# Kernel optimization log

Measured on AMD Instinct MI355X. Metric: run time of the kernel, lower is better.

## Reference

```python
import jax, jax.numpy as jnp
import numpy as np

N, E, C, Z, NB, NG, NL = 4000, 48000, 64, 10, 8, 8, 2
R_MAX = 5.0
P = 5.0  # polynomial cutoff power
AVG_NEIGH = 12.0
# l-index of each of the 16 spherical-harmonic components (l = 0..3)
ELLS = np.concatenate([[0], [1] * 3, [2] * 5, [3] * 7])


def _sph(u):
    # component-normalized real spherical harmonics up to l=3, u: unit vectors [E,3]
    x, y, z = u[..., 0], u[..., 1], u[..., 2]
    s3 = np.sqrt(3.0); s5 = np.sqrt(5.0); s15 = np.sqrt(15.0)
    s7 = np.sqrt(7.0); s105 = np.sqrt(105.0)
    s35_8 = np.sqrt(35.0 / 8.0); s21_8 = np.sqrt(21.0 / 8.0)
    x2, y2, z2 = x * x, y * y, z * z
    return jnp.stack([
        jnp.ones_like(x),
        s3 * x, s3 * y, s3 * z,
        s15 * x * y, s15 * y * z, 0.5 * s5 * (3.0 * z2 - 1.0), s15 * x * z, 0.5 * s15 * (x2 - y2),
        s35_8 * y * (3.0 * x2 - y2), s105 * x * y * z, s21_8 * y * (5.0 * z2 - 1.0),
        0.5 * s7 * z * (5.0 * z2 - 3.0), s21_8 * x * (5.0 * z2 - 1.0),
        0.5 * s105 * z * (x2 - y2), s35_8 * x * (x2 - 3.0 * y2),
    ], axis=-1)


def _radial(r):
    # Bessel radial basis * polynomial cutoff envelope; r: [E,1] -> [E,NB]
    n = jnp.arange(1, NB + 1, dtype=r.dtype)
    bess = np.sqrt(2.0 / R_MAX) * jnp.sin(n * jnp.pi * r / R_MAX) / r
    u = r / R_MAX
    env = 1.0 - 0.5 * (P + 1) * (P + 2) * u ** P + P * (P + 2) * u ** (P + 1) - 0.5 * P * (P + 1) * u ** (P + 2)
    env = jnp.where(u < 1.0, env, 0.0)
    return bess * env


def _per_l(f, W):
    # per-degree (l) channel mixing: f [N,C,16], W [4,C,C]
    return jnp.einsum('ncm,mcd->ndm', f, W[ELLS])


def _model(positions, x, shifts, W_embed, W_up, Wm1, Wm2, Wm3, W_out, W_sc, a_sc, w_poly, W_prod, w_r0, W_r1, w_r2, edge_index, batch):
    sender, receiver = edge_index[0], edge_index[1]
    vec = positions[receiver] - positions[sender] + shifts          # [E,3]
    length = jnp.sqrt(jnp.sum(vec * vec, axis=-1, keepdims=True))   # [E,1]
    edge_attrs = _sph(vec / length)                                 # [E,16]
    edge_feats = _radial(length)                                    # [E,NB]
    nf = jnp.zeros((N, C, 16), positions.dtype).at[:, :, 0].set(x @ W_embed)
    node_e = jnp.zeros((N,), positions.dtype)
    for i in range(NL):
        h = _per_l(nf, W_up[i])                                     # [N,C,16]
        w = jax.nn.silu(edge_feats @ Wm1[i])
        w = jax.nn.silu(w @ Wm2[i])
        w = (w @ Wm3[i]).reshape(E, C, 4)                           # per-(channel,l) radial weights
        h_s = h[:, :, 0][sender][:, :, None]                        # sender scalar feats [E,C,1]
        m = w[:, :, ELLS] * edge_attrs[:, None, :] * h_s            # messages [E,C,16]
        agg = jax.ops.segment_sum(m, receiver, num_segments=N) / AVG_NEIGH
        out = _per_l(agg, W_out[i])
        sc = _per_l(nf, W_sc[i]) * (x @ a_sc[i])[:, :, None]        # element-dependent skip
        s = out[:, :, 0]
        gate = w_poly[i, 0] + w_poly[i, 1] * s + w_poly[i, 2] * s * s  # correlation-3 scalar gate
        nf = _per_l(out * gate[:, :, None], W_prod[i]) + sc
        if i < NL - 1:
            node_e = node_e + nf[:, :, 0] @ w_r0
        else:
            node_e = node_e + jax.nn.silu(nf[:, :, 0] @ W_r1) @ w_r2
    snap = jax.ops.segment_sum(node_e, batch, num_segments=NG)
    return snap, node_e


def setup_inputs() -> dict:
    key = jax.random.key(0)
    ks = jax.random.split(key, 20)
    positions = jax.random.normal(ks[0], (N, 3), jnp.float32) * 3.0
    species = jax.random.randint(ks[1], (N,), 0, Z)
    x = jax.nn.one_hot(species, Z, dtype=jnp.float32)
    sender = jax.random.randint(ks[2], (E,), 0, N)
    offset = jax.random.randint(ks[3], (E,), 1, N)
    receiver = (sender + offset) % N  # no self loops -> length > 0
    edge_index = jnp.stack([sender, receiver]).astype(jnp.int32)
    shifts = jnp.zeros((E, 3), jnp.float32)
    batch = jnp.sort(jax.random.randint(ks[4], (N,), 0, NG)).astype(jnp.int32)
    g = lambda k, shp, scale: jax.random.normal(k, shp, jnp.float32) * scale
    inv = 1.0 / np.sqrt(C)
    return {
        'positions': positions, 'x': x, 'shifts': shifts,
        'W_embed': g(ks[5], (Z, C), 1.0 / np.sqrt(Z)),
        'W_up': g(ks[6], (NL, 4, C, C), inv),
        'Wm1': g(ks[7], (NL, NB, 64), 1.0 / np.sqrt(NB)),
        'Wm2': g(ks[8], (NL, 64, 64), 0.125),
        'Wm3': g(ks[9], (NL, 64, 4 * C), 0.125),
        'W_out': g(ks[10], (NL, 4, C, C), inv),
        'W_sc': g(ks[11], (NL, 4, C, C), inv),
        'a_sc': g(ks[12], (NL, Z, C), 1.0),
        'w_poly': g(ks[13], (NL, 3, C), 0.5),
        'W_prod': g(ks[14], (NL, 4, C, C), inv),
        'w_r0': g(ks[15], (C,), inv),
        'W_r1': g(ks[16], (C, 16), inv),
        'w_r2': g(ks[17], (16,), 0.25),
        'edge_index': edge_index, 'batch': batch,
    }


def reference(positions, x, shifts, W_embed, W_up, Wm1, Wm2, Wm3, W_out, W_sc, a_sc, w_poly, W_prod, w_r0, W_r1, w_r2, edge_index, batch):
    def efn(pos):
        snap, node_e = _model(pos, x, shifts, W_embed, W_up, Wm1, Wm2, Wm3, W_out, W_sc, a_sc, w_poly, W_prod, w_r0, W_r1, w_r2, edge_index, batch)
        return jnp.sum(snap), (snap, node_e)
    (_, (snap, node_e)), g = jax.value_and_grad(efn, has_aux=True)(positions)
    forces = -g
    return snap, node_e, forces
```

## Files before the change

kernel.cpp:

```cpp
#include <hip/hip_runtime.h>
#include <math.h>

constexpr int NN = 4000;
constexpr int EE = 48000;
constexpr int ZZ = 10;
constexpr float RMAX = 5.0f;
constexpr float INV_AVG = 1.0f / 12.0f;

constexpr int GB_EDGE = 188;
constexpr int GB_SPEC = GB_EDGE + 16;
constexpr int GB_W3Z  = GB_SPEC + 32;
constexpr int GB_T0   = GB_W3Z + 3;
constexpr int GB_ZERO = GB_T0 + 64;
constexpr int ZWS_F4  = 3*NN*64/4;
constexpr int ZOUT_F4 = 3*NN/4;

__device__ __forceinline__ float rl(float v, int lane){
    return __uint_as_float(__builtin_amdgcn_readlane(__float_as_uint(v), lane));
}
__device__ __forceinline__ float sigf(float x){ return 1.0f/(1.0f+__expf(-x)); }
__device__ __forceinline__ float siluf(float x){ return x*sigf(x); }
__device__ __forceinline__ float dsiluf(float x){ float s=sigf(x); return s*(1.0f+x*(1.0f-s)); }

__device__ __forceinline__ void pin64(float (&W)[64]){
#pragma unroll
    for (int i=0;i<64;i++) asm volatile("" : "+v"(W[i]));
}
__device__ __forceinline__ void pin8(float (&W)[8]){
#pragma unroll
    for (int i=0;i<8;i++) asm volatile("" : "+v"(W[i]));
}

__device__ __forceinline__ float bmv64(float src, const float (&W)[64]){
    float a0=0.f,a1=0.f,a2=0.f,a3=0.f;
#pragma unroll
    for (int k=0;k<64;k+=4){
        a0 += rl(src,k+0)*W[k+0];
        a1 += rl(src,k+1)*W[k+1];
        a2 += rl(src,k+2)*W[k+2];
        a3 += rl(src,k+3)*W[k+3];
    }
    return (a0+a1)+(a2+a3);
}
__device__ __forceinline__ void load_row64(const float* __restrict__ p, float (&W)[64]){
#pragma unroll
    for (int i=0;i<16;i++){
        float4 v = reinterpret_cast<const float4*>(p)[i];
        W[4*i]=v.x; W[4*i+1]=v.y; W[4*i+2]=v.z; W[4*i+3]=v.w;
    }
}
__device__ __forceinline__ void load_col64(const float* __restrict__ p, int lane, float (&W)[64]){
#pragma unroll
    for (int k=0;k<64;k++) W[k] = p[k*64+lane];
}

__global__ void k_zero(int* __restrict__ ecount, float* __restrict__ out)
{
    int t = threadIdx.x;
    if (t < 8) out[t] = 0.0f;
    if (t == 8) *ecount = 0;
}

__global__ void k_geom(const float* __restrict__ pos, const float* __restrict__ shifts,
                       const int* __restrict__ ei, const float* __restrict__ x,
                       const float* __restrict__ WE, const float* __restrict__ W_up,
                       const float* __restrict__ W_sc, const float* __restrict__ a_sc,
                       const float* __restrict__ Wm3,
                       int* __restrict__ spec,
                       float* __restrict__ u3c, float* __restrict__ frc, float* __restrict__ dfrc,
                       int* __restrict__ esrc, int* __restrict__ edst, int* __restrict__ ecount,
                       float* __restrict__ T0, float* __restrict__ SC0, float* __restrict__ W3z,
                       float4* __restrict__ zws, float* __restrict__ out)
{
    int b = blockIdx.x;
    if (b >= GB_T0){
        if (b >= GB_ZERO) return;
        if (b >= GB_W3Z && b < GB_T0){}
        if (b >= GB_T0 && b < GB_ZERO){
            float4 z4 = make_float4(0.f,0.f,0.f,0.f);
            float4* zout = (float4*)(out + 8 + NN);
            for (int i=(b-GB_T0)*256 + threadIdx.x; i < ZWS_F4 + ZOUT_F4; i += 64*256){
                if (i < ZWS_F4) zws[i] = z4;
                else zout[i-ZWS_F4] = z4;
            }
            return;
        }
    }
    if (b >= GB_W3Z && b < GB_T0){
        int wv = (b-GB_W3Z)*4 + (threadIdx.x>>6);
        int lane = threadIdx.x & 63;
        if (wv < ZZ){
            float wev = WE[wv*64 + lane];
            float t=0.f, sc=0.f;
#pragma unroll
            for (int c=0;c<64;c++){
                float w = rl(wev,c);
                t  += w*W_up[c*64+lane];
                sc += w*W_sc[c*64+lane];
            }
            T0[wv*64+lane]  = t;
            SC0[wv*64+lane] = sc * a_sc[wv*64+lane];
        }
        return;
    }
    if (b >= GB_SPEC && b < GB_W3Z){
        int idx = (b-GB_SPEC)*256 + threadIdx.x;
        int l = idx >> 12;
        int kc = idx & 4095;
        int k = kc >> 6, c = kc & 63;
        W3z[idx] = Wm3[l*64*256 + k*256 + 4*c];
        return;
    }
    if (b >= GB_EDGE){
        int n = (b-GB_EDGE)*256 + threadIdx.x;
        if (n < NN){
            int sp = 0;
#pragma unroll
            for (int j=0;j<ZZ;j++) if (x[n*ZZ+j] > 0.5f) sp = j;
            spec[n] = sp;
        }
        return;
    }
    int e = b*256 + threadIdx.x;
    if (e >= EE) return;
    int s = ei[e], r = ei[EE+e];
    float vx = pos[r*3+0]-pos[s*3+0]+shifts[e*3+0];
    float vy = pos[r*3+1]-pos[s*3+1]+shifts[e*3+1];
    float vz = pos[r*3+2]-pos[s*3+2]+shifts[e*3+2];
    float rr = sqrtf(vx*vx+vy*vy+vz*vz);
    float u = rr*(1.0f/RMAX);
    if (u >= 1.0f) return;
    int slot = atomicAdd(ecount, 1);
    esrc[slot]=s; edst[slot]=r;
    float inv = 1.0f/rr;
    u3c[slot*3+0]=vx*inv; u3c[slot*3+1]=vy*inv; u3c[slot*3+2]=vz*inv;
    float u2=u*u, u4=u2*u2, u5=u4*u;
    float env  = 1.0f - 21.0f*u5 + 35.0f*u5*u - 15.0f*u5*u2;
    float om   = 1.0f-u;
    float denv = -21.0f*u4*om*om;
    const float A = 0.6324555320336759f;
    const float K1 = 3.14159265358979f/RMAX;
    float a  = K1*rr;
    float s1 = __sinf(a), c1 = __cosf(a);
    float sp = 0.0f, cp = 1.0f, sn = s1, cn = c1;
#pragma unroll
    for (int n=1;n<=8;n++){
        float k = (float)n*K1;
        float bess  = A*sn*inv;
        float dbess = A*(k*cn - sn*inv)*inv;
        frc [slot*8+n-1] = bess*env;
        dfrc[slot*8+n-1] = dbess*env + bess*denv;
        float s2 = 2.0f*c1*sn - sp; sp=sn; sn=s2;
        float c2 = 2.0f*c1*cn - cp; cp=cn; cn=c2;
    }
}

template<int L>
__global__ __launch_bounds__(256,3)
void k_edge_fwd(const float* __restrict__ frc, const int* __restrict__ esrc,
                const int* __restrict__ edst, const int* __restrict__ ecount,
                const int* __restrict__ spec, const float* __restrict__ T0,
                const float* __restrict__ h1,
                const float* __restrict__ W1, const float* __restrict__ W2,
                const float* __restrict__ W3z,
                float* __restrict__ agg, float* __restrict__ t2b,
                float* __restrict__ w0b)
{
    int lane = threadIdx.x & 63;
    int wid  = __builtin_amdgcn_readfirstlane((blockIdx.x*256 + threadIdx.x) >> 6);
    const int nw = 512*4;
    int cnt  = ecount[0];
    float W1c[8], W2c[64], W3c[64];
#pragma unroll
    for (int j=0;j<8;j++) W1c[j] = W1[j*64+lane];
    load_col64(W2,  lane, W2c);
    load_col64(W3z, lane, W3c);
    pin8(W1c); pin64(W2c); pin64(W3c);
    for (int slot=wid; slot<cnt; slot+=nw){
        int us = __builtin_amdgcn_readfirstlane(slot);
        int s = esrc[us], r = edst[us];
        float fv = frc[us*8 + (lane&7)];
        float t1=0.f;
#pragma unroll
        for (int j=0;j<8;j++) t1 += rl(fv,j)*W1c[j];
        float a1v = siluf(t1);
        float t2  = bmv64(a1v, W2c);
        float a2v = siluf(t2);
        float w0  = bmv64(a2v, W3c);
        if (L==1){
            t2b[(size_t)us*64+lane] = t2;
            w0b[(size_t)us*64+lane] = w0;
        }
        float h = (L==0) ? T0[spec[s]*64+lane] : h1[s*64+lane];
        atomicAdd(&agg[r*64+lane], w0*h*INV_AVG);
    }
}

__global__ __launch_bounds__(256,2)
void k_node_fwd0(const float* __restrict__ agg, const float* __restrict__ SC0,
                 const int* __restrict__ spec, const int* __restrict__ batch,
                 const float* __restrict__ Wout, const float* __restrict__ Wprod,
                 const float* __restrict__ Wup1, const float* __restrict__ poly,
                 const float* __restrict__ wr0,
                 float* __restrict__ s0, float* __restrict__ nf1,
                 float* __restrict__ h1, float* __restrict__ out)
{
    __shared__ float part[8];
    if (threadIdx.x < 8) part[threadIdx.x] = 0.f;
    __syncthreads();
    int lane = threadIdx.x & 63;
    int wid = __builtin_amdgcn_readfirstlane((blockIdx.x*256 + threadIdx.x) >> 6);
    float WA[64], WB[64], WC[64];
    load_col64(Wout, lane, WA);
    load_col64(Wprod,lane, WB);
    load_col64(Wup1, lane, WC);
    pin64(WA); pin64(WB); pin64(WC);
    float p0=poly[lane], p1=poly[64+lane], p2=poly[128+lane];
    float w0r = wr0[lane];
#pragma unroll
    for (int i=0;i<4;i++){
        int n = wid + i*1000;
        float av = agg[n*64+lane];
        float s  = bmv64(av, WA);
        float gate = p0 + p1*s + p2*s*s;
        float nf = bmv64(s*gate, WB) + SC0[spec[n]*64+lane];
        s0 [n*64+lane] = s;
        nf1[n*64+lane] = nf;
        h1 [n*64+lane] = bmv64(nf, WC);
        float ne = nf*w0r;
#pragma unroll
        for (int off=32;off;off>>=1) ne += __shfl_xor(ne,off);
        if (lane==0){ out[8+n] = ne; atomicAdd(&part[batch[n]], ne); }
    }
    __syncthreads();
    if (threadIdx.x < 8) atomicAdd(&out[threadIdx.x], part[threadIdx.x]);
}

__global__ __launch_bounds__(256,2)
void k_node1(const float* __restrict__ agg, const float* __restrict__ nf1,
             const int* __restrict__ spec, const int* __restrict__ batch,
             const float* __restrict__ Wout, const float* __restrict__ Wprod,
             const float* __restrict__ Wsc, const float* __restrict__ asc,
             const float* __restrict__ poly, const float* __restrict__ Wr1,
             const float* __restrict__ wr2,
             float* __restrict__ out, float* __restrict__ gagg, float* __restrict__ gacc)
{
    __shared__ float part[8];
    if (threadIdx.x < 8) part[threadIdx.x] = 0.f;
    __syncthreads();
    int lane = threadIdx.x & 63;
    int wid = __builtin_amdgcn_readfirstlane((blockIdx.x*256 + threadIdx.x) >> 6);
    float WA[64], WB[64], WC[64];
    float sA[4], nfA[4], gA[4]; int spA[4];
    float p0=poly[lane], p1=poly[64+lane], p2=poly[128+lane];
    load_col64(Wout, lane, WA);
    load_col64(Wprod,lane, WB);
    load_col64(Wsc,  lane, WC);
    pin64(WA); pin64(WB); pin64(WC);
#pragma unroll
    for (int i=0;i<4;i++){
        int n = wid + i*1000;
        spA[i] = spec[n];
        float av  = agg[n*64+lane];
        float nfv = nf1[n*64+lane];
        float s   = bmv64(av, WA);
        float gate = p0 + p1*s + p2*s*s;
        float scp = bmv64(nfv, WC);
        sA[i]  = s;
        nfA[i] = bmv64(s*gate, WB) + scp*asc[spA[i]*64+lane];
    }
    int j = lane & 15;
    float w2 = wr2[j];
#pragma unroll
    for (int c=0;c<64;c++) WA[c] = Wr1[c*16 + j];
    pin64(WA);
#pragma unroll
    for (int i2=0;i2<4;i2++){
        float4 v = reinterpret_cast<const float4*>(Wr1 + lane*16)[i2];
        WC[4*i2]=v.x; WC[4*i2+1]=v.y; WC[4*i2+2]=v.z; WC[4*i2+3]=v.w;
    }
#pragma unroll
    for (int i=0;i<4;i++){
        int n = wid + i*1000;
        float z  = bmv64(nfA[i], WA);
        float ne = siluf(z)*w2;
#pragma unroll
        for (int off=32;off;off>>=1) ne += __shfl_xor(ne,off);
        ne *= 0.25f;
        float gz = w2*dsiluf(z);
        float g = 0.f;
#pragma unroll
        for (int jj=0;jj<16;jj++) g += rl(gz,jj)*WC[jj];
        gA[i] = g;
        if (lane==0){ out[8+n] += ne; atomicAdd(&part[batch[n]], ne); }
    }
    load_row64(Wprod + lane*64, WA);
    load_row64(Wout  + lane*64, WB);
    load_row64(Wsc   + lane*64, WC);
    pin64(WA); pin64(WB); pin64(WC);
#pragma unroll
    for (int i=0;i<4;i++){
        int n = wid + i*1000;
        float g  = gA[i];
        float gv = bmv64(g, WA);
        float s  = sA[i];
        float gate = p0 + p1*s + p2*s*s;
        float gs = gv*(gate + s*(p1 + 2.0f*p2*s));
        gagg[n*64+lane] = bmv64(gs, WB);
        gacc[n*64+lane] = bmv64(g*asc[spA[i]*64+lane], WC);
    }
    __syncthreads();
    if (threadIdx.x < 8) atomicAdd(&out[threadIdx.x], part[threadIdx.x]);
}

__global__ __launch_bounds__(256,2)
void k_bnode0(const float* __restrict__ ghb, const float* __restrict__ gacc,
              const float* __restrict__ Wup1, const float* __restrict__ wr0,
              const float* __restrict__ sbuf, const float* __restrict__ Wout,
              const float* __restrict__ Wprod, const float* __restrict__ poly,
              float* __restrict__ gagg)
{
    int lane = threadIdx.x & 63;
    int wid = __builtin_amdgcn_readfirstlane((blockIdx.x*256 + threadIdx.x) >> 6);
    float WA[64], WB[64], WC[64];
    load_row64(Wup1 + lane*64, WA);
    load_row64(Wprod+ lane*64, WB);
    load_row64(Wout + lane*64, WC);
    pin64(WA); pin64(WB); pin64(WC);
    float p0=poly[lane], p1=poly[64+lane], p2=poly[128+lane];
    float w0r = wr0[lane];
#pragma unroll
    for (int i=0;i<4;i++){
        int n = wid + i*1000;
        float gh = ghb[n*64+lane];
        float g  = bmv64(gh, WA) + gacc[n*64+lane] + w0r;
        float gv = bmv64(g, WB);
        float s  = sbuf[n*64+lane];
        float gate = p0 + p1*s + p2*s*s;
        float gs = gv*(gate + s*(p1 + 2.0f*p2*s));
        gagg[n*64+lane] = bmv64(gs, WC);
    }
}

__global__ __launch_bounds__(256,3)
void k_edge_bwd1(const float* __restrict__ frc, const float* __restrict__ dfrc,
                 const float* __restrict__ u3c, const int* __restrict__ esrc,
                 const int* __restrict__ edst, const int* __restrict__ ecount,
                 const float* __restrict__ h1, const float* __restrict__ gagg,
                 const float* __restrict__ t2b, const float* __restrict__ w0b,
                 const float* __restrict__ W1, const float* __restrict__ W2,
                 const float* __restrict__ W3z,
                 float* __restrict__ ghb, float* __restrict__ out)
{
    int lane = threadIdx.x & 63;
    int wid  = __builtin_amdgcn_readfirstlane((blockIdx.x*256 + threadIdx.x) >> 6);
    const int nw = 512*4;
    int cnt  = ecount[0];
    float* outf = out + 8 + NN;
    float W3r[64], W2r[64], W1c[8];
    load_row64(W3z + lane*64, W3r);
    load_row64(W2  + lane*64, W2r);
#pragma unroll
    for (int j=0;j<8;j++) W1c[j] = W1[j*64+lane];
    pin64(W3r); pin64(W2r); pin8(W1c);
    for (int slot=wid; slot<cnt; slot+=nw){
        int us = __builtin_amdgcn_readfirstlane(slot);
        int s = esrc[us], r = edst[us];
        float gm = gagg[r*64+lane]*INV_AVG;
        float h  = h1[s*64+lane];
        atomicAdd(&ghb[s*64+lane], gm*w0b[(size_t)us*64+lane]);
        float ga2 = bmv64(gm*h, W3r);
        float gt2 = ga2*dsiluf(t2b[(size_t)us*64+lane]);
        float ga1 = bmv64(gt2, W2r);
        float fv  = frc [us*8+(lane&7)];
        float dfv = dfrc[us*8+(lane&7)];
        float t1=0.f, wd=0.f;
#pragma unroll
        for (int j=0;j<8;j++){ t1 += rl(fv,j)*W1c[j]; wd += rl(dfv,j)*W1c[j]; }
        float p = ga1*dsiluf(t1)*wd;
#pragma unroll
        for (int off=32;off;off>>=1) p += __shfl_xor(p,off);
        if (lane<3) atomicAdd(&outf[r*3+lane], -u3c[us*3+lane]*p);
        else if (lane>=32 && lane<35){ int d=lane-32; atomicAdd(&outf[s*3+d], u3c[us*3+d]*p); }
    }
}

__global__ __launch_bounds__(256,2)
void k_edge_bwd0(const float* __restrict__ frc, const float* __restrict__ dfrc,
                 const float* __restrict__ u3c, const int* __restrict__ esrc,
                 const int* __restrict__ edst, const int* __restrict__ ecount,
                 const int* __restrict__ spec, const float* __restrict__ T0,
                 const float* __restrict__ gagg,
                 const float* __restrict__ W1, const float* __restrict__ W2,
                 const float* __restrict__ W3z,
                 float* __restrict__ out)
{
    int lane = threadIdx.x & 63;
    int wid  = __builtin_amdgcn_readfirstlane((blockIdx.x*256 + threadIdx.x) >> 6);
    const int nw = 512*4;
    int cnt  = ecount[0];
    float* outf = out + 8 + NN;
    float W3r[64], W2r[64], W2c[64], W1c[8];
    load_row64(W3z + lane*64, W3r);
    load_row64(W2  + lane*64, W2r);
    load_col64(W2, lane, W2c);
#pragma unroll
    for (int j=0;j<8;j++) W1c[j] = W1[j*64+lane];
    pin64(W3r); pin64(W2r); pin64(W2c); pin8(W1c);
    for (int slot=wid; slot<cnt; slot+=nw){
        int us = __builtin_amdgcn_readfirstlane(slot);
        int s = esrc[us], r = edst[us];
        float gm = gagg[r*64+lane]*INV_AVG;
        float h  = T0[spec[s]*64+lane];
        float ga2 = bmv64(gm*h, W3r);
        float fv  = frc [us*8+(lane&7)];
        float dfv = dfrc[us*8+(lane&7)];
        float t1=0.f, wd=0.f;
#pragma unroll
        for (int j=0;j<8;j++){ t1 += rl(fv,j)*W1c[j]; wd += rl(dfv,j)*W1c[j]; }
        float a1v = siluf(t1);
        float t2  = bmv64(a1v, W2c);
        float gt2 = ga2*dsiluf(t2);
        float ga1 = bmv64(gt2, W2r);
        float p = ga1*dsiluf(t1)*wd;
#pragma unroll
        for (int off=32;off;off>>=1) p += __shfl_xor(p,off);
        if (lane<3) atomicAdd(&outf[r*3+lane], -u3c[us*3+lane]*p);
        else if (lane>=32 && lane<35){ int d=lane-32; atomicAdd(&outf[s*3+d], u3c[us*3+d]*p); }
    }
}

extern "C" void kernel_launch(void* const* d_in, const int* in_sizes, int n_in,
                              void* d_out, int out_size, void* d_ws, size_t ws_size,
                              hipStream_t stream)
{
    (void)in_sizes; (void)n_in; (void)out_size; (void)ws_size;
    const float* pos    = (const float*)d_in[0];
    const float* x      = (const float*)d_in[1];
    const float* shifts = (const float*)d_in[2];
    const float* W_embed= (const float*)d_in[3];
    const float* W_up   = (const float*)d_in[4];
    const float* Wm1    = (const float*)d_in[5];
    const float* Wm2    = (const float*)d_in[6];
    const float* Wm3    = (const float*)d_in[7];
    const float* W_out  = (const float*)d_in[8];
    const float* W_sc   = (const float*)d_in[9];
    const float* a_sc   = (const float*)d_in[10];
    const float* w_poly = (const float*)d_in[11];
    const float* W_prod = (const float*)d_in[12];
    const float* w_r0   = (const float*)d_in[13];
    const float* W_r1   = (const float*)d_in[14];
    const float* w_r2   = (const float*)d_in[15];
    const int*   ei     = (const int*)d_in[16];
    const int*   batch  = (const int*)d_in[17];
    float* out = (float*)d_out;

    float* F = (float*)d_ws;
    float* agg0 = F; F += NN*64;
    float* agg1 = F; F += NN*64;
    float* ghb  = F; F += NN*64;
    int* ecount = (int*)F; F += 4;
    float* u3c  = F; F += 3*EE;
    float* frc  = F; F += 8*EE;
    float* dfrc = F; F += 8*EE;
    float* t2b1 = F; F += (size_t)EE*64;
    float* w0b1 = F; F += (size_t)EE*64;
    float* h1   = F; F += NN*64;
    float* nf1  = F; F += NN*64;
    float* s0   = F; F += NN*64;
    float* gagg1= F; F += NN*64;
    float* gagg0= F; F += NN*64;
    float* gacc = F; F += NN*64;
    float* T0   = F; F += ZZ*64;
    float* SC0  = F; F += ZZ*64;
    float* W3z  = F; F += 2*64*64;
    int* spec   = (int*)F; F += NN;
    int* esrc   = (int*)F; F += EE;
    int* edst   = (int*)F; F += EE;

    const float* U0 = W_up;           const float* U1 = W_up   + 4*64*64;
    const float* O0 = W_out;          const float* O1 = W_out  + 4*64*64;
    const float* S0w= W_sc;           const float* S1w= W_sc   + 4*64*64;
    const float* P0 = W_prod;         const float* P1 = W_prod + 4*64*64;
    const float* M1_0=Wm1,  *M1_1=Wm1+8*64;
    const float* M2_0=Wm2,  *M2_1=Wm2+64*64;
    const float* asc1=a_sc+ZZ*64;
    const float* pl0=w_poly, *pl1=w_poly+3*64;
    float* W3z0 = W3z; float* W3z1 = W3z + 64*64;

    k_zero<<<1, 256, 0, stream>>>(ecount, out);
    k_geom<<<GB_ZERO, 256, 0, stream>>>(pos, shifts, ei, x, W_embed, U0, S0w, a_sc, Wm3,
                                        spec, u3c, frc, dfrc, esrc, edst, ecount,
                                        T0, SC0, W3z, (float4*)d_ws, out);

    k_edge_fwd<0><<<512,256,0,stream>>>(frc, esrc, edst, ecount, spec, T0, nullptr,
                                        M1_0, M2_0, W3z0, agg0, nullptr, nullptr);
    k_node_fwd0<<<250,256,0,stream>>>(agg0, SC0, spec, batch, O0, P0, U1, pl0, w_r0,
                                      s0, nf1, h1, out);
    k_edge_fwd<1><<<512,256,0,stream>>>(frc, esrc, edst, ecount, spec, nullptr, h1,
                                        M1_1, M2_1, W3z1, agg1, t2b1, w0b1);
    k_node1<<<250,256,0,stream>>>(agg1, nf1, spec, batch, O1, P1, S1w, asc1, pl1,
                                  W_r1, w_r2, out, gagg1, gacc);

    k_edge_bwd1<<<512,256,0,stream>>>(frc, dfrc, u3c, esrc, edst, ecount, h1,
                                      gagg1, t2b1, w0b1, M1_1, M2_1, W3z1, ghb, out);
    k_bnode0<<<250,256,0,stream>>>(ghb, gacc, U1, w_r0, s0, O0, P0, pl0, gagg0);
    k_edge_bwd0<<<512,256,0,stream>>>(frc, dfrc, u3c, esrc, edst, ecount, spec, T0,
                                      gagg0, M1_0, M2_0, W3z0, out);
}
```

Before: 159.3 us.

## Fuse all stages into one persistent kernel with software grid barriers

Replaces the sequence of nine launches (geometry, two forward edge passes, node passes, backward edge and node passes) with a single persistent 512-block kernel. Stages are separated by atomic-counter grid barriers instead of kernel boundaries. The layer-0 t2 activations are now also stored so the backward pass can reuse them. This is meant to remove launch gaps and tail idle time between the many short stages. In exchange it relies on all 512 blocks being co-resident, forces launch bounds of 2 blocks per CU, and adds barrier spin cost and extra memory traffic for the stored activations.

```diff
diff --git a/kernel.cpp b/kernel.cpp
--- a/kernel.cpp
+++ b/kernel.cpp
@@ -7,11 +7,13 @@
 constexpr float RMAX = 5.0f;
 constexpr float INV_AVG = 1.0f / 12.0f;
 
-constexpr int GB_EDGE = 188;
-constexpr int GB_SPEC = GB_EDGE + 16;
-constexpr int GB_W3Z  = GB_SPEC + 32;
-constexpr int GB_T0   = GB_W3Z + 3;
-constexpr int GB_ZERO = GB_T0 + 64;
+constexpr int GRID  = 512;
+constexpr int NWAVE = GRID * 4;
+
+constexpr int RB_SPEC = 188;
+constexpr int RB_W3Z  = 204;
+constexpr int RB_T0   = 236;
+constexpr int RB_ZERO = 239;
 constexpr int ZWS_F4  = 3*NN*64/4;
 constexpr int ZOUT_F4 = 3*NN/4;
 
@@ -30,7 +32,6 @@
 #pragma unroll
     for (int i=0;i<8;i++) asm volatile("" : "+v"(W[i]));
 }
-
 __device__ __forceinline__ float bmv64(float src, const float (&W)[64]){
     float a0=0.f,a1=0.f,a2=0.f,a3=0.f;
 #pragma unroll
@@ -54,379 +55,375 @@
     for (int k=0;k<64;k++) W[k] = p[k*64+lane];
 }
 
-__global__ void k_zero(int* __restrict__ ecount, float* __restrict__ out)
+__device__ __forceinline__ void gbar(int* __restrict__ bc, int id){
+    __syncthreads();
+    if (threadIdx.x == 0){
+        __threadfence();
+        __hip_atomic_fetch_add(bc + id*64, 1, __ATOMIC_RELEASE, __HIP_MEMORY_SCOPE_AGENT);
+        while (__hip_atomic_load(bc + id*64, __ATOMIC_ACQUIRE, __HIP_MEMORY_SCOPE_AGENT) < GRID)
+            __builtin_amdgcn_s_sleep(1);
+        __threadfence();
+    }
+    __syncthreads();
+}
+
+__global__ void k_zero(int* __restrict__ barcnt, int* __restrict__ ecount, float* __restrict__ out)
 {
     int t = threadIdx.x;
+    barcnt[t] = 0; barcnt[t+256] = 0;
+    if (t == 0) *ecount = 0;
     if (t < 8) out[t] = 0.0f;
-    if (t == 8) *ecount = 0;
-}
-
-__global__ void k_geom(const float* __restrict__ pos, const float* __restrict__ shifts,
-                       const int* __restrict__ ei, const float* __restrict__ x,
-                       const float* __restrict__ WE, const float* __restrict__ W_up,
-                       const float* __restrict__ W_sc, const float* __restrict__ a_sc,
-                       const float* __restrict__ Wm3,
-                       int* __restrict__ spec,
-                       float* __restrict__ u3c, float* __restrict__ frc, float* __restrict__ dfrc,
-                       int* __restrict__ esrc, int* __restrict__ edst, int* __restrict__ ecount,
-                       float* __restrict__ T0, float* __restrict__ SC0, float* __restrict__ W3z,
-                       float4* __restrict__ zws, float* __restrict__ out)
+}
+
+__global__ __launch_bounds__(256,2)
+void k_main(const float* __restrict__ pos, const float* __restrict__ shifts,
+            const int* __restrict__ ei, const float* __restrict__ x,
+            const float* __restrict__ WE, const float* __restrict__ W_up,
+            const float* __restrict__ Wm1, const float* __restrict__ Wm2,
+            const float* __restrict__ Wm3, const float* __restrict__ W_out,
+            const float* __restrict__ W_sc, const float* __restrict__ a_sc,
+            const float* __restrict__ w_poly, const float* __restrict__ W_prod,
+            const float* __restrict__ w_r0, const float* __restrict__ W_r1,
+            const float* __restrict__ w_r2, const int* __restrict__ batch,
+            int* __restrict__ spec, float* __restrict__ u3c,
+            float* __restrict__ frc, float* __restrict__ dfrc,
+            int* __restrict__ esrc, int* __restrict__ edst, int* __restrict__ ecount,
+            float* __restrict__ T0, float* __restrict__ SC0, float* __restrict__ W3z,
+            float* __restrict__ agg0, float* __restrict__ agg1, float* __restrict__ ghb,
+            float* __restrict__ t2b0, float* __restrict__ t2b1, float* __restrict__ w0b1,
+            float* __restrict__ h1b, float* __restrict__ nf1b, float* __restrict__ s0b,
+            float* __restrict__ gagg0, float* __restrict__ gagg1, float* __restrict__ gacc,
+            int* __restrict__ barcnt, float4* __restrict__ zws,
+            float* __restrict__ out)
 {
-    int b = blockIdx.x;
-    if (b >= GB_T0){
-        if (b >= GB_ZERO) return;
-        if (b >= GB_W3Z && b < GB_T0){}
-        if (b >= GB_T0 && b < GB_ZERO){
-            float4 z4 = make_float4(0.f,0.f,0.f,0.f);
-            float4* zout = (float4*)(out + 8 + NN);
-            for (int i=(b-GB_T0)*256 + threadIdx.x; i < ZWS_F4 + ZOUT_F4; i += 64*256){
-                if (i < ZWS_F4) zws[i] = z4;
-                else zout[i-ZWS_F4] = z4;
+    __shared__ float part[8];
+    const int bid  = blockIdx.x;
+    const int tid  = threadIdx.x;
+    const int lane = tid & 63;
+    const int gw   = bid*4 + (tid>>6);
+
+    const float* U0  = W_up;          const float* U1  = W_up   + 16384;
+    const float* O0  = W_out;         const float* O1  = W_out  + 16384;
+    const float* S0w = W_sc;          const float* S1w = W_sc   + 16384;
+    const float* P0w = W_prod;        const float* P1w = W_prod + 16384;
+    const float* M1_0= Wm1;           const float* M1_1= Wm1 + 512;
+    const float* M2_0= Wm2;           const float* M2_1= Wm2 + 4096;
+    const float* asc1= a_sc + ZZ*64;
+    const float* pl0 = w_poly;        const float* pl1 = w_poly + 192;
+    const float* W3z0= W3z;           const float* W3z1= W3z + 4096;
+    float* outf = out + 8 + NN;
+
+    if (bid < RB_SPEC){
+        int e = bid*256 + tid;
+        if (e < EE){
+            int s = ei[e], r = ei[EE+e];
+            float vx = pos[r*3+0]-pos[s*3+0]+shifts[e*3+0];
+            float vy = pos[r*3+1]-pos[s*3+1]+shifts[e*3+1];
+            float vz = pos[r*3+2]-pos[s*3+2]+shifts[e*3+2];
+            float rr = sqrtf(vx*vx+vy*vy+vz*vz);
+            float u = rr*(1.0f/RMAX);
+            if (u < 1.0f){
+                int slot = atomicAdd(ecount, 1);
+                esrc[slot]=s; edst[slot]=r;
+                float inv = 1.0f/rr;
+                u3c[slot*3+0]=vx*inv; u3c[slot*3+1]=vy*inv; u3c[slot*3+2]=vz*inv;
+                float u2=u*u, u4=u2*u2, u5=u4*u;
+                float env  = 1.0f - 21.0f*u5 + 35.0f*u5*u - 15.0f*u5*u2;
+                float om   = 1.0f-u;
+                float denv = -21.0f*u4*om*om;
+                const float A  = 0.6324555320336759f;
+                const float K1 = 3.14159265358979f/RMAX;
+                float a  = K1*rr;
+                float s1 = __sinf(a), c1 = __cosf(a);
+                float sp = 0.0f, cp = 1.0f, sn = s1, cn = c1;
+#pragma unroll
+                for (int n=1;n<=8;n++){
+                    float k = (float)n*K1;
+                    float bess  = A*sn*inv;
+                    float dbess = A*(k*cn - sn*inv)*inv;
+                    frc [slot*8+n-1] = bess*env;
+                    dfrc[slot*8+n-1] = dbess*env + bess*denv;
+                    float s2 = 2.0f*c1*sn - sp; sp=sn; sn=s2;
+                    float c2 = 2.0f*c1*cn - cp; cp=cn; cn=c2;
+                }
             }
-            return;
-        }
-    }
-    if (b >= GB_W3Z && b < GB_T0){
-        int wv = (b-GB_W3Z)*4 + (threadIdx.x>>6);
-        int lane = threadIdx.x & 63;
+        }
+    } else if (bid < RB_W3Z){
+        int n = (bid-RB_SPEC)*256 + tid;
+        if (n < NN){
+            int sp = 0;
+#pragma unroll
+            for (int j=0;j<ZZ;j++) if (x[n*ZZ+j] > 0.5f) sp = j;
+            spec[n] = sp;
+        }
+    } else if (bid < RB_T0){
+        int idx = (bid-RB_W3Z)*256 + tid;
+        int l = idx >> 12, kc = idx & 4095;
+        int k = kc >> 6, c = kc & 63;
+        W3z[idx] = Wm3[l*64*256 + k*256 + 4*c];
+    } else if (bid < RB_ZERO){
+        int wv = (bid-RB_T0)*4 + (tid>>6);
         if (wv < ZZ){
             float wev = WE[wv*64 + lane];
             float t=0.f, sc=0.f;
 #pragma unroll
             for (int c=0;c<64;c++){
                 float w = rl(wev,c);
-                t  += w*W_up[c*64+lane];
-                sc += w*W_sc[c*64+lane];
+                t  += w*U0 [c*64+lane];
+                sc += w*S0w[c*64+lane];
             }
-            T0[wv*64+lane]  = t;
+            T0 [wv*64+lane] = t;
             SC0[wv*64+lane] = sc * a_sc[wv*64+lane];
         }
-        return;
-    }
-    if (b >= GB_SPEC && b < GB_W3Z){
-        int idx = (b-GB_SPEC)*256 + threadIdx.x;
-        int l = idx >> 12;
-        int kc = idx & 4095;
-        int k = kc >> 6, c = kc & 63;
-        W3z[idx] = Wm3[l*64*256 + k*256 + 4*c];
-        return;
-    }
-    if (b >= GB_EDGE){
-        int n = (b-GB_EDGE)*256 + threadIdx.x;
-        if (n < NN){
-            int sp = 0;
-#pragma unroll
-            for (int j=0;j<ZZ;j++) if (x[n*ZZ+j] > 0.5f) sp = j;
-            spec[n] = sp;
-        }
-        return;
-    }
-    int e = b*256 + threadIdx.x;
-    if (e >= EE) return;
-    int s = ei[e], r = ei[EE+e];
-    float vx = pos[r*3+0]-pos[s*3+0]+shifts[e*3+0];
-    float vy = pos[r*3+1]-pos[s*3+1]+shifts[e*3+1];
-    float vz = pos[r*3+2]-pos[s*3+2]+shifts[e*3+2];
-    float rr = sqrtf(vx*vx+vy*vy+vz*vz);
-    float u = rr*(1.0f/RMAX);
-    if (u >= 1.0f) return;
-    int slot = atomicAdd(ecount, 1);
-    esrc[slot]=s; edst[slot]=r;
-    float inv = 1.0f/rr;
-    u3c[slot*3+0]=vx*inv; u3c[slot*3+1]=vy*inv; u3c[slot*3+2]=vz*inv;
-    float u2=u*u, u4=u2*u2, u5=u4*u;
-    float env  = 1.0f - 21.0f*u5 + 35.0f*u5*u - 15.0f*u5*u2;
-    float om   = 1.0f-u;
-    float denv = -21.0f*u4*om*om;
-    const float A = 0.6324555320336759f;
-    const float K1 = 3.14159265358979f/RMAX;
-    float a  = K1*rr;
-    float s1 = __sinf(a), c1 = __cosf(a);
-    float sp = 0.0f, cp = 1.0f, sn = s1, cn = c1;
-#pragma unroll
-    for (int n=1;n<=8;n++){
-        float k = (float)n*K1;
-        float bess  = A*sn*inv;
-        float dbess = A*(k*cn - sn*inv)*inv;
-        frc [slot*8+n-1] = bess*env;
-        dfrc[slot*8+n-1] = dbess*env + bess*denv;
-        float s2 = 2.0f*c1*sn - sp; sp=sn; sn=s2;
-        float c2 = 2.0f*c1*cn - cp; cp=cn; cn=c2;
-    }
-}
-
-template<int L>
-__global__ __launch_bounds__(256,3)
-void k_edge_fwd(const float* __restrict__ frc, const int* __restrict__ esrc,
-                const int* __restrict__ edst, const int* __restrict__ ecount,
-                const int* __restrict__ spec, const float* __restrict__ T0,
-                const float* __restrict__ h1,
-                const float* __restrict__ W1, const float* __restrict__ W2,
-                const float* __restrict__ W3z,
-                float* __restrict__ agg, float* __restrict__ t2b,
-                float* __restrict__ w0b)
-{
-    int lane = threadIdx.x & 63;
-    int wid  = __builtin_amdgcn_readfirstlane((blockIdx.x*256 + threadIdx.x) >> 6);
-    const int nw = 512*4;
-    int cnt  = ecount[0];
-    float W1c[8], W2c[64], W3c[64];
-#pragma unroll
-    for (int j=0;j<8;j++) W1c[j] = W1[j*64+lane];
-    load_col64(W2,  lane, W2c);
-    load_col64(W3z, lane, W3c);
-    pin8(W1c); pin64(W2c); pin64(W3c);
-    for (int slot=wid; slot<cnt; slot+=nw){
-        int us = __builtin_amdgcn_readfirstlane(slot);
-        int s = esrc[us], r = edst[us];
-        float fv = frc[us*8 + (lane&7)];
-        float t1=0.f;
-#pragma unroll
-        for (int j=0;j<8;j++) t1 += rl(fv,j)*W1c[j];
-        float a1v = siluf(t1);
-        float t2  = bmv64(a1v, W2c);
-        float a2v = siluf(t2);
-        float w0  = bmv64(a2v, W3c);
-        if (L==1){
-            t2b[(size_t)us*64+lane] = t2;
-            w0b[(size_t)us*64+lane] = w0;
-        }
-        float h = (L==0) ? T0[spec[s]*64+lane] : h1[s*64+lane];
-        atomicAdd(&agg[r*64+lane], w0*h*INV_AVG);
-    }
-}
-
-__global__ __launch_bounds__(256,2)
-void k_node_fwd0(const float* __restrict__ agg, const float* __restrict__ SC0,
-                 const int* __restrict__ spec, const int* __restrict__ batch,
-                 const float* __restrict__ Wout, const float* __restrict__ Wprod,
-                 const float* __restrict__ Wup1, const float* __restrict__ poly,
-                 const float* __restrict__ wr0,
-                 float* __restrict__ s0, float* __restrict__ nf1,
-                 float* __restrict__ h1, float* __restrict__ out)
-{
-    __shared__ float part[8];
-    if (threadIdx.x < 8) part[threadIdx.x] = 0.f;
-    __syncthreads();
-    int lane = threadIdx.x & 63;
-    int wid = __builtin_amdgcn_readfirstlane((blockIdx.x*256 + threadIdx.x) >> 6);
-    float WA[64], WB[64], WC[64];
-    load_col64(Wout, lane, WA);
-    load_col64(Wprod,lane, WB);
-    load_col64(Wup1, lane, WC);
-    pin64(WA); pin64(WB); pin64(WC);
-    float p0=poly[lane], p1=poly[64+lane], p2=poly[128+lane];
-    float w0r = wr0[lane];
-#pragma unroll
-    for (int i=0;i<4;i++){
-        int n = wid + i*1000;
-        float av = agg[n*64+lane];
-        float s  = bmv64(av, WA);
-        float gate = p0 + p1*s + p2*s*s;
-        float nf = bmv64(s*gate, WB) + SC0[spec[n]*64+lane];
-        s0 [n*64+lane] = s;
-        nf1[n*64+lane] = nf;
-        h1 [n*64+lane] = bmv64(nf, WC);
-        float ne = nf*w0r;
-#pragma unroll
-        for (int off=32;off;off>>=1) ne += __shfl_xor(ne,off);
-        if (lane==0){ out[8+n] = ne; atomicAdd(&part[batch[n]], ne); }
-    }
-    __syncthreads();
-    if (threadIdx.x < 8) atomicAdd(&out[threadIdx.x], part[threadIdx.x]);
-}
-
-__global__ __launch_bounds__(256,2)
-void k_node1(const float* __restrict__ agg, const float* __restrict__ nf1,
-             const int* __restrict__ spec, const int* __restrict__ batch,
-             const float* __restrict__ Wout, const float* __restrict__ Wprod,
-             const float* __restrict__ Wsc, const float* __restrict__ asc,
-             const float* __restrict__ poly, const float* __restrict__ Wr1,
-             const float* __restrict__ wr2,
-             float* __restrict__ out, float* __restrict__ gagg, float* __restrict__ gacc)
-{
-    __shared__ float part[8];
-    if (threadIdx.x < 8) part[threadIdx.x] = 0.f;
-    __syncthreads();
-    int lane = threadIdx.x & 63;
-    int wid = __builtin_amdgcn_readfirstlane((blockIdx.x*256 + threadIdx.x) >> 6);
-    float WA[64], WB[64], WC[64];
-    float sA[4], nfA[4], gA[4]; int spA[4];
-    float p0=poly[lane], p1=poly[64+lane], p2=poly[128+lane];
-    load_col64(Wout, lane, WA);
-    load_col64(Wprod,lane, WB);
-    load_col64(Wsc,  lane, WC);
-    pin64(WA); pin64(WB); pin64(WC);
-#pragma unroll
-    for (int i=0;i<4;i++){
-        int n = wid + i*1000;
-        spA[i] = spec[n];
-        float av  = agg[n*64+lane];
-        float nfv = nf1[n*64+lane];
-        float s   = bmv64(av, WA);
-        float gate = p0 + p1*s + p2*s*s;
-        float scp = bmv64(nfv, WC);
-        sA[i]  = s;
-        nfA[i] = bmv64(s*gate, WB) + scp*asc[spA[i]*64+lane];
-    }
-    int j = lane & 15;
-    float w2 = wr2[j];
-#pragma unroll
-    for (int c=0;c<64;c++) WA[c] = Wr1[c*16 + j];
-    pin64(WA);
-#pragma unroll
-    for (int i2=0;i2<4;i2++){
-        float4 v = reinterpret_cast<const float4*>(Wr1 + lane*16)[i2];
-        WC[4*i2]=v.x; WC[4*i2+1]=v.y; WC[4*i2+2]=v.z; WC[4*i2+3]=v.w;
-    }
-#pragma unroll
-    for (int i=0;i<4;i++){
-        int n = wid + i*1000;
-        float z  = bmv64(nfA[i], WA);
-        float ne = siluf(z)*w2;
-#pragma unroll
-        for (int off=32;off;off>>=1) ne += __shfl_xor(ne,off);
-        ne *= 0.25f;
-        float gz = w2*dsiluf(z);
-        float g = 0.f;
-#pragma unroll
-        for (int jj=0;jj<16;jj++) g += rl(gz,jj)*WC[jj];
-        gA[i] = g;
-        if (lane==0){ out[8+n] += ne; atomicAdd(&part[batch[n]], ne); }
-    }
-    load_row64(Wprod + lane*64, WA);
-    load_row64(Wout  + lane*64, WB);
-    load_row64(Wsc   + lane*64, WC);
-    pin64(WA); pin64(WB); pin64(WC);
-#pragma unroll
-    for (int i=0;i<4;i++){
-        int n = wid + i*1000;
-        float g  = gA[i];
-        float gv = bmv64(g, WA);
-        float s  = sA[i];
-        float gate = p0 + p1*s + p2*s*s;
-        float gs = gv*(gate + s*(p1 + 2.0f*p2*s));
-        gagg[n*64+lane] = bmv64(gs, WB);
-        gacc[n*64+lane] = bmv64(g*asc[spA[i]*64+lane], WC);
-    }
-    __syncthreads();
-    if (threadIdx.x < 8) atomicAdd(&out[threadIdx.x], part[threadIdx.x]);
-}
-
-__global__ __launch_bounds__(256,2)
-void k_bnode0(const float* __restrict__ ghb, const float* __restrict__ gacc,
-              const float* __restrict__ Wup1, const float* __restrict__ wr0,
-              const float* __restrict__ sbuf, const float* __restrict__ Wout,
-              const float* __restrict__ Wprod, const float* __restrict__ poly,
-              float* __restrict__ gagg)
-{
-    int lane = threadIdx.x & 63;
-    int wid = __builtin_amdgcn_readfirstlane((blockIdx.x*256 + threadIdx.x) >> 6);
-    float WA[64], WB[64], WC[64];
-    load_row64(Wup1 + lane*64, WA);
-    load_row64(Wprod+ lane*64, WB);
-    load_row64(Wout + lane*64, WC);
-    pin64(WA); pin64(WB); pin64(WC);
-    float p0=poly[lane], p1=poly[64+lane], p2=poly[128+lane];
-    float w0r = wr0[lane];
-#pragma unroll
-    for (int i=0;i<4;i++){
-        int n = wid + i*1000;
-        float gh = ghb[n*64+lane];
-        float g  = bmv64(gh, WA) + gacc[n*64+lane] + w0r;
-        float gv = bmv64(g, WB);
-        float s  = sbuf[n*64+lane];
-        float gate = p0 + p1*s + p2*s*s;
-        float gs = gv*(gate + s*(p1 + 2.0f*p2*s));
-        gagg[n*64+lane] = bmv64(gs, WC);
-    }
-}
-
-__global__ __launch_bounds__(256,3)
-void k_edge_bwd1(const float* __restrict__ frc, const float* __restrict__ dfrc,
-                 const float* __restrict__ u3c, const int* __restrict__ esrc,
-                 const int* __restrict__ edst, const int* __restrict__ ecount,
-                 const float* __restrict__ h1, const float* __restrict__ gagg,
-                 const float* __restrict__ t2b, const float* __restrict__ w0b,
-                 const float* __restrict__ W1, const float* __restrict__ W2,
-                 const float* __restrict__ W3z,
-                 float* __restrict__ ghb, float* __restrict__ out)
-{
-    int lane = threadIdx.x & 63;
-    int wid  = __builtin_amdgcn_readfirstlane((blockIdx.x*256 + threadIdx.x) >> 6);
-    const int nw = 512*4;
-    int cnt  = ecount[0];
-    float* outf = out + 8 + NN;
-    float W3r[64], W2r[64], W1c[8];
-    load_row64(W3z + lane*64, W3r);
-    load_row64(W2  + lane*64, W2r);
-#pragma unroll
-    for (int j=0;j<8;j++) W1c[j] = W1[j*64+lane];
-    pin64(W3r); pin64(W2r); pin8(W1c);
-    for (int slot=wid; slot<cnt; slot+=nw){
-        int us = __builtin_amdgcn_readfirstlane(slot);
-        int s = esrc[us], r = edst[us];
-        float gm = gagg[r*64+lane]*INV_AVG;
-        float h  = h1[s*64+lane];
-        atomicAdd(&ghb[s*64+lane], gm*w0b[(size_t)us*64+lane]);
-        float ga2 = bmv64(gm*h, W3r);
-        float gt2 = ga2*dsiluf(t2b[(size_t)us*64+lane]);
-        float ga1 = bmv64(gt2, W2r);
-        float fv  = frc [us*8+(lane&7)];
-        float dfv = dfrc[us*8+(lane&7)];
-        float t1=0.f, wd=0.f;
-#pragma unroll
-        for (int j=0;j<8;j++){ t1 += rl(fv,j)*W1c[j]; wd += rl(dfv,j)*W1c[j]; }
-        float p = ga1*dsiluf(t1)*wd;
-#pragma unroll
-        for (int off=32;off;off>>=1) p += __shfl_xor(p,off);
-        if (lane<3) atomicAdd(&outf[r*3+lane], -u3c[us*3+lane]*p);
-        else if (lane>=32 && lane<35){ int d=lane-32; atomicAdd(&outf[s*3+d], u3c[us*3+d]*p); }
-    }
-}
-
-__global__ __launch_bounds__(256,2)
-void k_edge_bwd0(const float* __restrict__ frc, const float* __restrict__ dfrc,
-                 const float* __restrict__ u3c, const int* __restrict__ esrc,
-                 const int* __restrict__ edst, const int* __restrict__ ecount,
-                 const int* __restrict__ spec, const float* __restrict__ T0,
-                 const float* __restrict__ gagg,
-                 const float* __restrict__ W1, const float* __restrict__ W2,
-                 const float* __restrict__ W3z,
-                 float* __restrict__ out)
-{
-    int lane = threadIdx.x & 63;
-    int wid  = __builtin_amdgcn_readfirstlane((blockIdx.x*256 + threadIdx.x) >> 6);
-    const int nw = 512*4;
-    int cnt  = ecount[0];
-    float* outf = out + 8 + NN;
-    float W3r[64], W2r[64], W2c[64], W1c[8];
-    load_row64(W3z + lane*64, W3r);
-    load_row64(W2  + lane*64, W2r);
-    load_col64(W2, lane, W2c);
-#pragma unroll
-    for (int j=0;j<8;j++) W1c[j] = W1[j*64+lane];
-    pin64(W3r); pin64(W2r); pin64(W2c); pin8(W1c);
-    for (int slot=wid; slot<cnt; slot+=nw){
-        int us = __builtin_amdgcn_readfirstlane(slot);
-        int s = esrc[us], r = edst[us];
-        float gm = gagg[r*64+lane]*INV_AVG;
-        float h  = T0[spec[s]*64+lane];
-        float ga2 = bmv64(gm*h, W3r);
-        float fv  = frc [us*8+(lane&7)];
-        float dfv = dfrc[us*8+(lane&7)];
-        float t1=0.f, wd=0.f;
-#pragma unroll
-        for (int j=0;j<8;j++){ t1 += rl(fv,j)*W1c[j]; wd += rl(dfv,j)*W1c[j]; }
-        float a1v = siluf(t1);
-        float t2  = bmv64(a1v, W2c);
-        float gt2 = ga2*dsiluf(t2);
-        float ga1 = bmv64(gt2, W2r);
-        float p = ga1*dsiluf(t1)*wd;
-#pragma unroll
-        for (int off=32;off;off>>=1) p += __shfl_xor(p,off);
-        if (lane<3) atomicAdd(&outf[r*3+lane], -u3c[us*3+lane]*p);
-        else if (lane>=32 && lane<35){ int d=lane-32; atomicAdd(&outf[s*3+d], u3c[us*3+d]*p); }
+    } else {
+        float4 z4 = make_float4(0.f,0.f,0.f,0.f);
+        float4* zout = (float4*)outf;
+        for (int i=(bid-RB_ZERO)*256 + tid; i < ZWS_F4 + ZOUT_F4; i += (GRID-RB_ZERO)*256){
+            if (i < ZWS_F4) zws[i] = z4;
+            else zout[i-ZWS_F4] = z4;
+        }
+    }
+    gbar(barcnt, 0);
+
+    {
+        float W1c[8], W2c[64], W3c[64];
+#pragma unroll
+        for (int j=0;j<8;j++) W1c[j] = M1_0[j*64+lane];
+        load_col64(M2_0, lane, W2c);
+        load_col64(W3z0, lane, W3c);
+        pin8(W1c); pin64(W2c); pin64(W3c);
+        int cnt = ecount[0];
+        for (int slot=gw; slot<cnt; slot+=NWAVE){
+            int s = esrc[slot], r = edst[slot];
+            float fv = frc[slot*8 + (lane&7)];
+            float t1=0.f;
+#pragma unroll
+            for (int j=0;j<8;j++) t1 += rl(fv,j)*W1c[j];
+            float t2 = bmv64(siluf(t1), W2c);
+            t2b0[(size_t)slot*64+lane] = t2;
+            float w0 = bmv64(siluf(t2), W3c);
+            float h  = T0[spec[s]*64+lane];
+            atomicAdd(&agg0[r*64+lane], w0*h*INV_AVG);
+        }
+    }
+    gbar(barcnt, 1);
+
+    {
+        if (tid < 8) part[tid] = 0.f;
+        __syncthreads();
+        float WA[64], WB[64], WC[64];
+        load_col64(O0,  lane, WA);
+        load_col64(P0w, lane, WB);
+        load_col64(U1,  lane, WC);
+        pin64(WA); pin64(WB); pin64(WC);
+        float p0=pl0[lane], p1=pl0[64+lane], p2=pl0[128+lane];
+        float w0r = w_r0[lane];
+        for (int n=gw; n<NN; n+=NWAVE){
+            float av = agg0[n*64+lane];
+            float s  = bmv64(av, WA);
+            float gate = p0 + p1*s + p2*s*s;
+            float nf = bmv64(s*gate, WB) + SC0[spec[n]*64+lane];
+            s0b [n*64+lane] = s;
+            nf1b[n*64+lane] = nf;
+            h1b [n*64+lane] = bmv64(nf, WC);
+            float ne = nf*w0r;
+#pragma unroll
+            for (int off=32;off;off>>=1) ne += __shfl_xor(ne,off);
+            if (lane==0){ out[8+n] = ne; atomicAdd(&part[batch[n]], ne); }
+        }
+        __syncthreads();
+        if (tid < 8) atomicAdd(&out[tid], part[tid]);
+    }
+    gbar(barcnt, 2);
+
+    {
+        float W1c[8], W2c[64], W3c[64];
+#pragma unroll
+        for (int j=0;j<8;j++) W1c[j] = M1_1[j*64+lane];
+        load_col64(M2_1, lane, W2c);
+        load_col64(W3z1, lane, W3c);
+        pin8(W1c); pin64(W2c); pin64(W3c);
+        int cnt = ecount[0];
+        for (int slot=gw; slot<cnt; slot+=NWAVE){
+            int s = esrc[slot], r = edst[slot];
+            float fv = frc[slot*8 + (lane&7)];
+            float t1=0.f;
+#pragma unroll
+            for (int j=0;j<8;j++) t1 += rl(fv,j)*W1c[j];
+            float t2 = bmv64(siluf(t1), W2c);
+            t2b1[(size_t)slot*64+lane] = t2;
+            float w0 = bmv64(siluf(t2), W3c);
+            w0b1[(size_t)slot*64+lane] = w0;
+            float h  = h1b[s*64+lane];
+            atomicAdd(&agg1[r*64+lane], w0*h*INV_AVG);
+        }
+    }
+    gbar(barcnt, 3);
+
+    {
+        if (tid < 8) part[tid] = 0.f;
+        __syncthreads();
+        float WA[64], WB[64], WC[64];
+        float p0=pl1[lane], p1=pl1[64+lane], p2=pl1[128+lane];
+        int na = gw, nb = gw + NWAVE;
+        bool vb = nb < NN;
+        int spa = spec[na], spb = vb ? spec[nb] : 0;
+        float sA, sB=0.f, nfA, nfB=0.f, gA, gB=0.f;
+        load_col64(O1,  lane, WA);
+        load_col64(P1w, lane, WB);
+        load_col64(S1w, lane, WC);
+        pin64(WA); pin64(WB); pin64(WC);
+        {
+            float av  = agg1[na*64+lane];
+            float nfv = nf1b[na*64+lane];
+            sA = bmv64(av, WA);
+            float gate = p0 + p1*sA + p2*sA*sA;
+            nfA = bmv64(sA*gate, WB) + bmv64(nfv, WC)*asc1[spa*64+lane];
+        }
+        if (vb){
+            float av  = agg1[nb*64+lane];
+            float nfv = nf1b[nb*64+lane];
+            sB = bmv64(av, WA);
+            float gate = p0 + p1*sB + p2*sB*sB;
+            nfB = bmv64(sB*gate, WB) + bmv64(nfv, WC)*asc1[spb*64+lane];
+        }
+        {
+            int j = lane & 15;
+            float w2 = w_r2[j];
+#pragma unroll
+            for (int c=0;c<64;c++) WA[c] = W_r1[c*16 + j];
+            pin64(WA);
+            float WR[16];
+#pragma unroll
+            for (int i2=0;i2<4;i2++){
+                float4 v = reinterpret_cast<const float4*>(W_r1 + lane*16)[i2];
+                WR[4*i2]=v.x; WR[4*i2+1]=v.y; WR[4*i2+2]=v.z; WR[4*i2+3]=v.w;
+            }
+            {
+                float z  = bmv64(nfA, WA);
+                float ne = siluf(z)*w2;
+#pragma unroll
+                for (int off=32;off;off>>=1) ne += __shfl_xor(ne,off);
+                ne *= 0.25f;
+                float gz = w2*dsiluf(z);
+                float g = 0.f;
+#pragma unroll
+                for (int jj=0;jj<16;jj++) g += rl(gz,jj)*WR[jj];
+                gA = g;
+                if (lane==0){ out[8+na] += ne; atomicAdd(&part[batch[na]], ne); }
+            }
+            if (vb){
+                float z  = bmv64(nfB, WA);
+                float ne = siluf(z)*w2;
+#pragma unroll
+                for (int off=32;off;off>>=1) ne += __shfl_xor(ne,off);
+                ne *= 0.25f;
+                float gz = w2*dsiluf(z);
+                float g = 0.f;
+#pragma unroll
+                for (int jj=0;jj<16;jj++) g += rl(gz,jj)*WR[jj];
+                gB = g;
+                if (lane==0){ out[8+nb] += ne; atomicAdd(&part[batch[nb]], ne); }
+            }
+        }
+        load_row64(P1w + lane*64, WA);
+        load_row64(O1  + lane*64, WB);
+        load_row64(S1w + lane*64, WC);
+        pin64(WA); pin64(WB); pin64(WC);
+        {
+            float gv = bmv64(gA, WA);
+            float gate = p0 + p1*sA + p2*sA*sA;
+            float gs = gv*(gate + sA*(p1 + 2.0f*p2*sA));
+            gagg1[na*64+lane] = bmv64(gs, WB);
+            gacc [na*64+lane] = bmv64(gA*asc1[spa*64+lane], WC);
+        }
+        if (vb){
+            float gv = bmv64(gB, WA);
+            float gate = p0 + p1*sB + p2*sB*sB;
+            float gs = gv*(gate + sB*(p1 + 2.0f*p2*sB));
+            gagg1[nb*64+lane] = bmv64(gs, WB);
+            gacc [nb*64+lane] = bmv64(gB*asc1[spb*64+lane], WC);
+        }
+        __syncthreads();
+        if (tid < 8) atomicAdd(&out[tid], part[tid]);
+    }
+    gbar(barcnt, 4);
+
+    {
+        float W3r[64], W2r[64], W1c[8];
+        load_row64(W3z1 + lane*64, W3r);
+        load_row64(M2_1 + lane*64, W2r);
+#pragma unroll
+        for (int j=0;j<8;j++) W1c[j] = M1_1[j*64+lane];
+        pin64(W3r); pin64(W2r); pin8(W1c);
+        int cnt = ecount[0];
+        for (int slot=gw; slot<cnt; slot+=NWAVE){
+            int s = esrc[slot], r = edst[slot];
+            float gm = gagg1[r*64+lane]*INV_AVG;
+            float h  = h1b[s*64+lane];
+            atomicAdd(&ghb[s*64+lane], gm*w0b1[(size_t)slot*64+lane]);
+            float ga2 = bmv64(gm*h, W3r);
+            float gt2 = ga2*dsiluf(t2b1[(size_t)slot*64+lane]);
+            float ga1 = bmv64(gt2, W2r);
+            float fv  = frc [slot*8+(lane&7)];
+            float dfv = dfrc[slot*8+(lane&7)];
+            float t1=0.f, wd=0.f;
+#pragma unroll
+            for (int j=0;j<8;j++){ t1 += rl(fv,j)*W1c[j]; wd += rl(dfv,j)*W1c[j]; }
+            float p = ga1*dsiluf(t1)*wd;
+#pragma unroll
+            for (int off=32;off;off>>=1) p += __shfl_xor(p,off);
+            if (lane<3) atomicAdd(&outf[r*3+lane], -u3c[slot*3+lane]*p);
+            else if (lane>=32 && lane<35){ int d=lane-32; atomicAdd(&outf[s*3+d], u3c[slot*3+d]*p); }
+        }
+    }
+    gbar(barcnt, 5);
+
+    {
+        float WA[64], WB[64], WC[64];
+        load_row64(U1  + lane*64, WA);
+        load_row64(P0w + lane*64, WB);
+        load_row64(O0  + lane*64, WC);
+        pin64(WA); pin64(WB); pin64(WC);
+        float p0=pl0[lane], p1=pl0[64+lane], p2=pl0[128+lane];
+        float w0r = w_r0[lane];
+        for (int n=gw; n<NN; n+=NWAVE){
+            float g  = bmv64(ghb[n*64+lane], WA) + gacc[n*64+lane] + w0r;
+            float gv = bmv64(g, WB);
+            float s  = s0b[n*64+lane];
+            float gate = p0 + p1*s + p2*s*s;
+            float gs = gv*(gate + s*(p1 + 2.0f*p2*s));
+            gagg0[n*64+lane] = bmv64(gs, WC);
+        }
+    }
+    gbar(barcnt, 6);
+
+    {
+        float W3r[64], W2r[64], W1c[8];
+        load_row64(W3z0 + lane*64, W3r);
+        load_row64(M2_0 + lane*64, W2r);
+#pragma unroll
+        for (int j=0;j<8;j++) W1c[j] = M1_0[j*64+lane];
+        pin64(W3r); pin64(W2r); pin8(W1c);
+        int cnt = ecount[0];
+        for (int slot=gw; slot<cnt; slot+=NWAVE){
+            int s = esrc[slot], r = edst[slot];
+            float gm = gagg0[r*64+lane]*INV_AVG;
+            float h  = T0[spec[s]*64+lane];
+            float ga2 = bmv64(gm*h, W3r);
+            float gt2 = ga2*dsiluf(t2b0[(size_t)slot*64+lane]);
+            float ga1 = bmv64(gt2, W2r);
+            float fv  = frc [slot*8+(lane&7)];
+            float dfv = dfrc[slot*8+(lane&7)];
+            float t1=0.f, wd=0.f;
+#pragma unroll
+            for (int j=0;j<8;j++){ t1 += rl(fv,j)*W1c[j]; wd += rl(dfv,j)*W1c[j]; }
+            float p = ga1*dsiluf(t1)*wd;
+#pragma unroll
+            for (int off=32;off;off>>=1) p += __shfl_xor(p,off);
+            if (lane<3) atomicAdd(&outf[r*3+lane], -u3c[slot*3+lane]*p);
+            else if (lane>=32 && lane<35){ int d=lane-32; atomicAdd(&outf[s*3+d], u3c[slot*3+d]*p); }
+        }
     }
 }
 
@@ -459,15 +456,15 @@
     float* agg0 = F; F += NN*64;
     float* agg1 = F; F += NN*64;
     float* ghb  = F; F += NN*64;
-    int* ecount = (int*)F; F += 4;
     float* u3c  = F; F += 3*EE;
     float* frc  = F; F += 8*EE;
     float* dfrc = F; F += 8*EE;
+    float* t2b0 = F; F += (size_t)EE*64;
     float* t2b1 = F; F += (size_t)EE*64;
     float* w0b1 = F; F += (size_t)EE*64;
-    float* h1   = F; F += NN*64;
-    float* nf1  = F; F += NN*64;
-    float* s0   = F; F += NN*64;
+    float* h1b  = F; F += NN*64;
+    float* nf1b = F; F += NN*64;
+    float* s0b  = F; F += NN*64;
     float* gagg1= F; F += NN*64;
     float* gagg0= F; F += NN*64;
     float* gacc = F; F += NN*64;
@@ -477,34 +474,14 @@
     int* spec   = (int*)F; F += NN;
     int* esrc   = (int*)F; F += EE;
     int* edst   = (int*)F; F += EE;
-
-    const float* U0 = W_up;           const float* U1 = W_up   + 4*64*64;
-    const float* O0 = W_out;          const float* O1 = W_out  + 4*64*64;
-    const float* S0w= W_sc;           const float* S1w= W_sc   + 4*64*64;
-    const float* P0 = W_prod;         const float* P1 = W_prod + 4*64*64;
-    const float* M1_0=Wm1,  *M1_1=Wm1+8*64;
-    const float* M2_0=Wm2,  *M2_1=Wm2+64*64;
-    const float* asc1=a_sc+ZZ*64;
-    const float* pl0=w_poly, *pl1=w_poly+3*64;
-    float* W3z0 = W3z; float* W3z1 = W3z + 64*64;
-
-    k_zero<<<1, 256, 0, stream>>>(ecount, out);
-    k_geom<<<GB_ZERO, 256, 0, stream>>>(pos, shifts, ei, x, W_embed, U0, S0w, a_sc, Wm3,
-                                        spec, u3c, frc, dfrc, esrc, edst, ecount,
-                                        T0, SC0, W3z, (float4*)d_ws, out);
-
-    k_edge_fwd<0><<<512,256,0,stream>>>(frc, esrc, edst, ecount, spec, T0, nullptr,
-                                        M1_0, M2_0, W3z0, agg0, nullptr, nullptr);
-    k_node_fwd0<<<250,256,0,stream>>>(agg0, SC0, spec, batch, O0, P0, U1, pl0, w_r0,
-                                      s0, nf1, h1, out);
-    k_edge_fwd<1><<<512,256,0,stream>>>(frc, esrc, edst, ecount, spec, nullptr, h1,
-                                        M1_1, M2_1, W3z1, agg1, t2b1, w0b1);
-    k_node1<<<250,256,0,stream>>>(agg1, nf1, spec, batch, O1, P1, S1w, asc1, pl1,
-                                  W_r1, w_r2, out, gagg1, gacc);
-
-    k_edge_bwd1<<<512,256,0,stream>>>(frc, dfrc, u3c, esrc, edst, ecount, h1,
-                                      gagg1, t2b1, w0b1, M1_1, M2_1, W3z1, ghb, out);
-    k_bnode0<<<250,256,0,stream>>>(ghb, gacc, U1, w_r0, s0, O0, P0, pl0, gagg0);
-    k_edge_bwd0<<<512,256,0,stream>>>(frc, dfrc, u3c, esrc, edst, ecount, spec, T0,
-                                      gagg0, M1_0, M2_0, W3z0, out);
-}
+    int* ecount = (int*)F; F += 4;
+    int* barcnt = (int*)F; F += 512;
+
+    k_zero<<<1, 256, 0, stream>>>(barcnt, ecount, out);
+    k_main<<<GRID, 256, 0, stream>>>(pos, shifts, ei, x, W_embed, W_up, Wm1, Wm2, Wm3,
+                                     W_out, W_sc, a_sc, w_poly, W_prod, w_r0, W_r1, w_r2,
+                                     batch, spec, u3c, frc, dfrc, esrc, edst, ecount,
+                                     T0, SC0, W3z, agg0, agg1, ghb, t2b0, t2b1, w0b1,
+                                     h1b, nf1b, s0b, gagg0, gagg1, gacc,
+                                     barcnt, (float4*)d_ws, out);
+}
```

Result: slower. 635.1 us (+298.8%).
